# Kernel tuning notes

Hardware: AMD Instinct MI355X
Metric: run time of the kernel (lower is better)

Reference implementation:

```python
import jax, jax.numpy as jnp
import numpy as np

IGNORE = -100000.0


def setup_inputs() -> dict:
    key = jax.random.key(0)
    ks = jax.random.split(key, 5)
    b, s, d_model = 4, 2048, 2048
    n_q, n_kv, d_head = 32, 8, 64
    std = 0.02
    return {
        "normalized_resid_pre": jax.random.normal(ks[0], (b, s, d_model), jnp.float32),
        "W_Q": jax.random.normal(ks[1], (n_q, d_model, d_head), jnp.float32) * std,
        "W_K": jax.random.normal(ks[2], (n_kv, d_model, d_head), jnp.float32) * std,
        "W_V": jax.random.normal(ks[3], (n_kv, d_model, d_head), jnp.float32) * std,
        "W_O": jax.random.normal(ks[4], (n_kv, d_head, d_model), jnp.float32) * std,
    }


def reference(normalized_resid_pre, W_Q, W_K, W_V, W_O):
    x = normalized_resid_pre
    b, s, _ = x.shape
    n_kv, d_head = W_K.shape[0], W_K.shape[2]
    n_q = W_Q.shape[0]
    g = n_q // n_kv

    q = jnp.einsum("bpd,hdk->bphk", x, W_Q)  # [b,s,n_q,d_head]
    k = jnp.einsum("bpd,ndk->bpnk", x, W_K)  # [b,s,n_kv,d_head]
    v = jnp.einsum("bpd,ndk->bpnk", x, W_V)  # [b,s,n_kv,d_head]

    # rearrange: head axis splits as (n_kv_heads, g_size), then moved to [b,s,g,n_kv,d_head]
    gq = q.reshape(b, s, n_kv, g, d_head).transpose(0, 1, 3, 2, 4)

    # NOTE: faithful to source — g axis is SUMMED in this einsum
    scores = jnp.einsum("bqgnh,bknh->bnqk", gq, k) / jnp.sqrt(jnp.float32(d_head))

    causal = jnp.triu(jnp.ones((s, s), dtype=bool), k=1)  # True above diagonal
    scores = jnp.where(causal, IGNORE, scores)
    pattern = jax.nn.softmax(scores, axis=-1)  # [b,n_kv,q,k]

    z = jnp.einsum("bknh,bnqk->bqnh", v, pattern)  # [b,s,n_kv,d_head]
    attn_out = jnp.einsum("bqnh,nhd->bqd", z, W_O)  # [b,s,d_model]
    return attn_out
```

## Files before the change

### kernel.cpp

```cpp
#include <hip/hip_runtime.h>

typedef __attribute__((ext_vector_type(8))) _Float16 half8;
typedef __attribute__((ext_vector_type(4))) float f32x4;

#define BATCH  4
#define SLEN   2048
#define DMODEL 2048
#define NKV    8
#define GRP    4
#define DH     64
#define QKV    1536
#define KVDIM  512
#define MROWS  (BATCH * SLEN)

__device__ __forceinline__ unsigned short f2h(float f) {
    union { _Float16 h; unsigned short u; } cv;
    cv.h = (_Float16)f;
    return cv.u;
}

__device__ __forceinline__ void gl16(const void* g, void* l) {
    __builtin_amdgcn_global_load_lds(
        (const __attribute__((address_space(1))) void*)g,
        (__attribute__((address_space(3))) void*)l, 16, 0, 0);
}

typedef __attribute__((ext_vector_type(4))) short short4v;
union U64S4 { unsigned long long u; short4v s; };

__global__ __launch_bounds__(256) void k_packT(const float* __restrict__ wq,
                                               const float* __restrict__ wk,
                                               const float* __restrict__ wv,
                                               unsigned short* __restrict__ outT) {
    __shared__ float T[64][65];
    const int d0 = blockIdx.x * 64;
    const int ct = blockIdx.y;
    const int mat = ct >> 3, n = ct & 7;
    const int tr = threadIdx.x >> 6, tc = threadIdx.x & 63;
#pragma unroll
    for (int i = 0; i < 16; ++i) {
        int row = tr + i * 4;
        float v;
        if (mat == 0) {
            v = 0.0f;
#pragma unroll
            for (int g = 0; g < GRP; ++g)
                v += wq[((size_t)(n * GRP + g) * DMODEL + d0 + row) * DH + tc];
        } else if (mat == 1) {
            v = wk[((size_t)n * DMODEL + d0 + row) * DH + tc];
        } else {
            v = wv[((size_t)n * DMODEL + d0 + row) * DH + tc];
        }
        T[row][tc] = v;
    }
    __syncthreads();
    const int rr = tc;
#pragma unroll
    for (int i = 0; i < 16; ++i) {
        int cc = tr + i * 4;
        outT[(size_t)(mat * 512 + n * 64 + cc) * DMODEL + d0 + rr] = f2h(T[rr][cc]);
    }
}

__global__ __launch_bounds__(256) void k_transconv_h(const float* __restrict__ in,
                                                     unsigned short* __restrict__ outT,
                                                     int R, int C) {
    __shared__ float T[64][65];
    const int r0 = blockIdx.x * 64, c0 = blockIdx.y * 64;
    const int tr = threadIdx.x >> 6, tc = threadIdx.x & 63;
#pragma unroll
    for (int i = 0; i < 16; ++i)
        T[tr + i * 4][tc] = in[(size_t)(r0 + tr + i * 4) * C + c0 + tc];
    __syncthreads();
    const int rr = tc;
#pragma unroll
    for (int i = 0; i < 16; ++i) {
        int cc = tr + i * 4;
        outT[(size_t)(c0 + cc) * R + r0 + rr] = f2h(T[rr][cc]);
    }
}

__global__ __launch_bounds__(256) void k_convh(const float* __restrict__ in,
                                               unsigned short* __restrict__ out,
                                               int n4) {
    int i = blockIdx.x * 256 + threadIdx.x;
    if (i >= n4) return;
    float4 v = ((const float4*)in)[i];
    ushort4 o;
    o.x = f2h(v.x); o.y = f2h(v.y); o.z = f2h(v.z); o.w = f2h(v.w);
    ((ushort4*)out)[i] = o;
}

__device__ __forceinline__ void stage_rows(const unsigned short* __restrict__ src,
                                           unsigned short* lds, int t, int K,
                                           int k0, int nslots4) {
#pragma unroll
    for (int j = 0; j < 8; ++j) {
        if (j >= nslots4) break;
        int slot = j * 256 + t;
        int row = slot >> 3, blk = slot & 7;
        int c = blk ^ (row & 7);
        gl16(src + (size_t)row * K + k0 + c * 8, lds + slot * 8);
    }
}

__global__ __launch_bounds__(256) void k_gemm_qkv(
        const unsigned short* __restrict__ Ag, const unsigned short* __restrict__ Bg,
        unsigned short* __restrict__ qk, unsigned short* __restrict__ vT) {
    __shared__ unsigned short A2[2][128 * 64];
    __shared__ unsigned short B2[2][192 * 64];

    const int t = threadIdx.x;
    const size_t m0 = (size_t)blockIdx.x * 128, n0 = (size_t)blockIdx.y * 192;
    const int w = t >> 6, l = t & 63;
    const int wm = (w >> 1) * 64, wn = (w & 1) * 96;
    const int r = l & 15, q = l >> 4;
    f32x4 acc[4][6] = {};
    const int K = DMODEL;
    const int NT = K / 64;

    stage_rows(Ag + m0 * K, A2[0], t, K, 0, 4);
    stage_rows(Bg + n0 * K, B2[0], t, K, 0, 6);
    asm volatile("s_waitcnt vmcnt(0)" ::: "memory");
    __builtin_amdgcn_s_barrier();
    int cur = 0;
    for (int kt = 0; kt < NT; ++kt) {
        if (kt + 1 < NT) {
            stage_rows(Ag + m0 * K, A2[cur ^ 1], t, K, (kt + 1) * 64, 4);
            stage_rows(Bg + n0 * K, B2[cur ^ 1], t, K, (kt + 1) * 64, 6);
        }
        const unsigned short* Ac = A2[cur];
        const unsigned short* Bc = B2[cur];
        half8 af[4][2], bf[6][2];
#pragma unroll
        for (int i = 0; i < 4; ++i)
#pragma unroll
            for (int ks = 0; ks < 2; ++ks) {
                int ra = wm + i * 16 + r;
                af[i][ks] = *(const half8*)&Ac[ra * 64 + ((((ks << 2) | q) ^ (ra & 7)) << 3)];
            }
#pragma unroll
        for (int j = 0; j < 6; ++j)
#pragma unroll
            for (int ks = 0; ks < 2; ++ks) {
                int rb = wn + j * 16 + r;
                bf[j][ks] = *(const half8*)&Bc[rb * 64 + ((((ks << 2) | q) ^ (rb & 7)) << 3)];
            }
        __builtin_amdgcn_s_setprio(1);
#pragma unroll
        for (int i = 0; i < 4; ++i)
#pragma unroll
            for (int j = 0; j < 6; ++j) {
                acc[i][j] = __builtin_amdgcn_mfma_f32_16x16x32_f16(af[i][0], bf[j][0], acc[i][j], 0, 0, 0);
                acc[i][j] = __builtin_amdgcn_mfma_f32_16x16x32_f16(af[i][1], bf[j][1], acc[i][j], 0, 0, 0);
            }
        __builtin_amdgcn_s_setprio(0);
        asm volatile("s_waitcnt vmcnt(0)" ::: "memory");
        __builtin_amdgcn_s_barrier();
        cur ^= 1;
    }

#pragma unroll
    for (int i = 0; i < 4; ++i)
#pragma unroll
        for (int j = 0; j < 6; ++j) {
            int col = (int)n0 + wn + j * 16 + r;
            size_t rowb = m0 + wm + i * 16 + q * 4;
            if (col < 1024) {
#pragma unroll
                for (int e = 0; e < 4; ++e)
                    qk[(rowb + e) * 1024 + col] = f2h(acc[i][j][e]);
            } else {
                int d = col - 1024;
                ushort4 pk;
                pk.x = f2h(acc[i][j][0]); pk.y = f2h(acc[i][j][1]);
                pk.z = f2h(acc[i][j][2]); pk.w = f2h(acc[i][j][3]);
                *(ushort4*)&vT[(size_t)d * MROWS + rowb] = pk;
            }
        }
}

__global__ __launch_bounds__(256) void k_gemm_out(
        const unsigned short* __restrict__ Ag, const unsigned short* __restrict__ Bg,
        float* __restrict__ C) {
    __shared__ unsigned short A2[2][128 * 64];
    __shared__ unsigned short B2[2][128 * 64];

    const int t = threadIdx.x;
    const size_t m0 = (size_t)blockIdx.x * 128, n0 = (size_t)blockIdx.y * 128;
    const int w = t >> 6, l = t & 63;
    const int wm = (w >> 1) * 64, wn = (w & 1) * 64;
    const int r = l & 15, q = l >> 4;
    f32x4 acc[4][4] = {};
    const int K = KVDIM;
    const int NT = K / 64;

    stage_rows(Ag + m0 * K, A2[0], t, K, 0, 4);
    stage_rows(Bg + n0 * K, B2[0], t, K, 0, 4);
    asm volatile("s_waitcnt vmcnt(0)" ::: "memory");
    __builtin_amdgcn_s_barrier();
    int cur = 0;
    for (int kt = 0; kt < NT; ++kt) {
        if (kt + 1 < NT) {
            stage_rows(Ag + m0 * K, A2[cur ^ 1], t, K, (kt + 1) * 64, 4);
            stage_rows(Bg + n0 * K, B2[cur ^ 1], t, K, (kt + 1) * 64, 4);
        }
        const unsigned short* Ac = A2[cur];
        const unsigned short* Bc = B2[cur];
        half8 af[4][2], bf[4][2];
#pragma unroll
        for (int i = 0; i < 4; ++i)
#pragma unroll
            for (int ks = 0; ks < 2; ++ks) {
                int ra = wm + i * 16 + r;
                af[i][ks] = *(const half8*)&Ac[ra * 64 + ((((ks << 2) | q) ^ (ra & 7)) << 3)];
                int rb = wn + i * 16 + r;
                bf[i][ks] = *(const half8*)&Bc[rb * 64 + ((((ks << 2) | q) ^ (rb & 7)) << 3)];
            }
        __builtin_amdgcn_s_setprio(1);
#pragma unroll
        for (int i = 0; i < 4; ++i)
#pragma unroll
            for (int j = 0; j < 4; ++j) {
                acc[i][j] = __builtin_amdgcn_mfma_f32_16x16x32_f16(af[i][0], bf[j][0], acc[i][j], 0, 0, 0);
                acc[i][j] = __builtin_amdgcn_mfma_f32_16x16x32_f16(af[i][1], bf[j][1], acc[i][j], 0, 0, 0);
            }
        __builtin_amdgcn_s_setprio(0);
        asm volatile("s_waitcnt vmcnt(0)" ::: "memory");
        __builtin_amdgcn_s_barrier();
        cur ^= 1;
    }

#pragma unroll
    for (int i = 0; i < 4; ++i)
#pragma unroll
        for (int j = 0; j < 4; ++j) {
            int col = (int)n0 + wn + j * 16 + r;
            size_t rowb = m0 + wm + i * 16 + q * 4;
#pragma unroll
            for (int e = 0; e < 4; ++e)
                C[(rowb + e) * DMODEL + col] = acc[i][j][e];
        }
}

__global__ __launch_bounds__(256) void k_attn_mfma(
        const unsigned short* __restrict__ qk, const unsigned short* __restrict__ vT,
        unsigned short* __restrict__ zh) {
    __shared__ unsigned short Ks[2][128 * 64];
    __shared__ unsigned short Vs[2][64 * 128];
    __shared__ unsigned short Pt[4 * 128 * 16];

    const int t  = threadIdx.x;
    const int w  = t >> 6, l = t & 63;
    const int p  = blockIdx.x;
    const int n  = blockIdx.y, b = blockIdx.z;
    const int r  = l & 15, g = l >> 4;
    const int wq0 = w * 16;

#define STAGE_KV(buf, kr0)                                                    \
    _Pragma("unroll") for (int j2 = 0; j2 < 4; ++j2) {                        \
        int s2 = j2 * 256 + t;                                                \
        int rK = s2 >> 3, cK = (s2 & 7) ^ (rK & 7);                           \
        gl16(qk + ((kr0) + rK) * 1024 + 512 + n * 64 + cK * 8,                \
             &Ks[buf][s2 * 8]);                                               \
        int rV = s2 >> 4, cV = (s2 & 15) ^ (rV & 15);                         \
        gl16(vT + (size_t)(n * 64 + rV) * MROWS + (kr0) + cV * 8,             \
             &Vs[buf][s2 * 8]);                                               \
    }

#pragma unroll 1
    for (int seg = 0; seg < 2; ++seg) {
        const int qt = seg ? p : (31 - p);
        const int nkt = (qt + 2) >> 1;
        const size_t qrow0 = (size_t)(b * SLEN + qt * 64);

        half8 qh[2];
#pragma unroll
        for (int ks = 0; ks < 2; ++ks) {
            size_t off = (qrow0 + wq0 + r) * 1024 + n * 64 + ks * 32 + g * 8;
            qh[ks] = *(const half8*)(qk + off);
#pragma unroll
            for (int e2 = 0; e2 < 8; ++e2) qh[ks][e2] = qh[ks][e2] * (_Float16)0.125f;
        }

        STAGE_KV(0, (size_t)(b * SLEN))
        asm volatile("s_waitcnt vmcnt(0)" ::: "memory");
        __builtin_amdgcn_s_barrier();

        float m_[4], lsum[4];
#pragma unroll
        for (int e = 0; e < 4; ++e) { m_[e] = -3.0e38f; lsum[e] = 0.0f; }
        f32x4 accz[4] = {};

        for (int kt = 0; kt < nkt; ++kt) {
            const int cur = kt & 1;
            if (kt + 1 < nkt) {
                STAGE_KV(cur ^ 1, (size_t)(b * SLEN + (kt + 1) * 128))
            }
            const unsigned short* Ksc = Ks[cur];
            const unsigned short* Vsc = Vs[cur];

            f32x4 s[8] = {};
#pragma unroll
            for (int ct = 0; ct < 8; ++ct)
#pragma unroll
                for (int ks = 0; ks < 2; ++ks) {
                    int row = ct * 16 + r;
                    int off = row * 128 + (((ks * 4 + g) ^ (row & 7)) << 4);
                    half8 kh8 = *(const half8*)((char*)Ksc + off);
                    s[ct] = __builtin_amdgcn_mfma_f32_16x16x32_f16(qh[ks], kh8, s[ct], 0, 0, 0);
                }

            if (kt == nkt - 1) {
#pragma unroll
                for (int ct = 0; ct < 8; ++ct)
#pragma unroll
                    for (int e = 0; e < 4; ++e)
                        if ((kt * 128 + ct * 16 + r) > (qt * 64 + wq0 + g * 4 + e))
                            s[ct][e] = -100000.0f;
            }

            float al[4], nm[4];
#pragma unroll
            for (int e = 0; e < 4; ++e) {
                float pm = fmaxf(fmaxf(fmaxf(s[0][e], s[1][e]), fmaxf(s[2][e], s[3][e])),
                                 fmaxf(fmaxf(s[4][e], s[5][e]), fmaxf(s[6][e], s[7][e])));
                pm = fmaxf(pm, __shfl_xor(pm, 1));
                pm = fmaxf(pm, __shfl_xor(pm, 2));
                pm = fmaxf(pm, __shfl_xor(pm, 4));
                pm = fmaxf(pm, __shfl_xor(pm, 8));
                nm[e] = fmaxf(m_[e], pm);
                al[e] = __expf(m_[e] - nm[e]);
                m_[e] = nm[e];
            }
            {
                int src = (r >> 2) << 4;
                float a0 = __shfl(al[0], src), a1 = __shfl(al[1], src);
                float a2 = __shfl(al[2], src), a3 = __shfl(al[3], src);
                float ax = (r & 1) ? a1 : a0, ay = (r & 1) ? a3 : a2;
                float aq = (r & 2) ? ay : ax;
#pragma unroll
                for (int dt = 0; dt < 4; ++dt) {
                    accz[dt][0] *= aq; accz[dt][1] *= aq;
                    accz[dt][2] *= aq; accz[dt][3] *= aq;
                }
            }

            float ps[4] = {};
#pragma unroll
            for (int ct = 0; ct < 8; ++ct) {
                float p0 = __expf(s[ct][0] - m_[0]);
                float p1 = __expf(s[ct][1] - m_[1]);
                float p2 = __expf(s[ct][2] - m_[2]);
                float p3 = __expf(s[ct][3] - m_[3]);
                ps[0] += p0; ps[1] += p1; ps[2] += p2; ps[3] += p3;
                short4v pk = { (short)f2h(p0), (short)f2h(p1),
                               (short)f2h(p2), (short)f2h(p3) };
                int kv = ct * 16 + r;
                int phys = (kv >> 5) * 32 + (((kv >> 2) & 1) << 4)
                         + (((kv >> 3) & 3) << 2) + (kv & 3);
                *(short4v*)((char*)Pt + w * 4096 + phys * 32 + g * 8) = pk;
            }

#pragma unroll
            for (int e = 0; e < 4; ++e) {
                float rs = ps[e];
                rs += __shfl_xor(rs, 1); rs += __shfl_xor(rs, 2);
                rs += __shfl_xor(rs, 4); rs += __shfl_xor(rs, 8);
                lsum[e] = lsum[e] * al[e] + rs;
            }

            asm volatile("s_waitcnt lgkmcnt(0)" ::: "memory");
            __builtin_amdgcn_sched_barrier(0);
            U64S4 tA[4], tB[4];
#pragma unroll
            for (int ks = 0; ks < 4; ++ks) {
                unsigned base = (unsigned)(size_t)((char*)Pt + w * 4096 + ks * 1024) + l * 8;
                asm volatile("ds_read_b64_tr_b16 %0, %1" : "=v"(tA[ks].u) : "v"(base) : "memory");
                asm volatile("ds_read_b64_tr_b16 %0, %1" : "=v"(tB[ks].u) : "v"(base + 512) : "memory");
            }
            asm volatile("s_waitcnt lgkmcnt(0)" ::: "memory");
            __builtin_amdgcn_sched_barrier(0);
#pragma unroll
            for (int ks = 0; ks < 4; ++ks) {
                union { short s[8]; half8 h; } pf;
                pf.s[0] = tA[ks].s[0]; pf.s[1] = tA[ks].s[1];
                pf.s[2] = tA[ks].s[2]; pf.s[3] = tA[ks].s[3];
                pf.s[4] = tB[ks].s[0]; pf.s[5] = tB[ks].s[1];
                pf.s[6] = tB[ks].s[2]; pf.s[7] = tB[ks].s[3];
#pragma unroll
                for (int dt = 0; dt < 4; ++dt) {
                    int d = dt * 16 + r;
                    int off = d * 256 + (((ks * 4 + g) ^ (d & 15)) << 4);
                    half8 vfrag = *(const half8*)((char*)Vsc + off);
                    accz[dt] = __builtin_amdgcn_mfma_f32_16x16x32_f16(vfrag, pf.h, accz[dt], 0, 0, 0);
                }
            }

            asm volatile("s_waitcnt vmcnt(0)" ::: "memory");
            __builtin_amdgcn_s_barrier();
        }

        int src = (r >> 2) << 4;
        float l0 = __shfl(lsum[0], src), l1 = __shfl(lsum[1], src);
        float l2 = __shfl(lsum[2], src), l3 = __shfl(lsum[3], src);
        float lx = (r & 1) ? l1 : l0, ly = (r & 1) ? l3 : l2;
        float inv = 1.0f / ((r & 2) ? ly : lx);
#pragma unroll
        for (int dt = 0; dt < 4; ++dt) {
            ushort4 h4;
#pragma unroll
            for (int e = 0; e < 4; ++e)
                ((unsigned short*)&h4)[e] = f2h(accz[dt][e] * inv);
            size_t off = (qrow0 + wq0 + r) * 512 + n * 64 + dt * 16 + g * 4;
            *(ushort4*)(zh + off) = h4;
        }
    }
#undef STAGE_KV
}

extern "C" void kernel_launch(void* const* d_in, const int* in_sizes, int n_in,
                              void* d_out, int out_size, void* d_ws, size_t ws_size,
                              hipStream_t stream) {
    const float* x  = (const float*)d_in[0];
    const float* wq = (const float*)d_in[1];
    const float* wk = (const float*)d_in[2];
    const float* wv = (const float*)d_in[3];
    const float* wo = (const float*)d_in[4];
    float* out = (float*)d_out;

    char* w = (char*)d_ws;
    unsigned short* xh  = (unsigned short*)(w);
    unsigned short* zh  = (unsigned short*)(w);
    unsigned short* qk  = (unsigned short*)(w + 33554432);
    unsigned short* vT  = (unsigned short*)(w + 50331648);
    unsigned short* wcatT = (unsigned short*)(w + 58720256);
    unsigned short* woT = (unsigned short*)(w + 65011712);

    k_packT<<<dim3(32, 24), 256, 0, stream>>>(wq, wk, wv, wcatT);
    k_transconv_h<<<dim3(8, 32), 256, 0, stream>>>(wo, woT, KVDIM, DMODEL);
    k_convh<<<dim3(16384), 256, 0, stream>>>(x, xh, MROWS * DMODEL / 4);
    k_gemm_qkv<<<dim3(64, 8), 256, 0, stream>>>(xh, wcatT, qk, vT);
    k_attn_mfma<<<dim3(16, NKV, BATCH), 256, 0, stream>>>(qk, vT, zh);
    k_gemm_out<<<dim3(64, 16), 256, 0, stream>>>(zh, woT, out);
}
```

Before: 188.2 us.

## Double query rows per attention block to reuse staged K/V tiles

The attention kernel now processes 128 query rows per block instead of 64, with each wave handling two 16-row query slices against the same K/V tiles in LDS. This halves K/V staging traffic and barriers per query row, and the grid is halved to match. In exchange it doubles accumulator and score registers per wave, grows the P staging buffer, restricts occupancy to one block per SIMD set via launch bounds, and leaves fewer blocks for load balancing under the causal mask.

After: 200.5 us. +6.5%, slower.

```diff
diff --git a/kernel.cpp b/kernel.cpp
--- a/kernel.cpp
+++ b/kernel.cpp
@@ -243,19 +243,18 @@
         }
 }
 
-__global__ __launch_bounds__(256) void k_attn_mfma(
+__global__ __launch_bounds__(256, 1) void k_attn_mfma(
         const unsigned short* __restrict__ qk, const unsigned short* __restrict__ vT,
         unsigned short* __restrict__ zh) {
     __shared__ unsigned short Ks[2][128 * 64];
     __shared__ unsigned short Vs[2][64 * 128];
-    __shared__ unsigned short Pt[4 * 128 * 16];
+    __shared__ unsigned short Pt[4 * 2 * 2048];
 
     const int t  = threadIdx.x;
     const int w  = t >> 6, l = t & 63;
     const int p  = blockIdx.x;
     const int n  = blockIdx.y, b = blockIdx.z;
     const int r  = l & 15, g = l >> 4;
-    const int wq0 = w * 16;
 
 #define STAGE_KV(buf, kr0)                                                    \
     _Pragma("unroll") for (int j2 = 0; j2 < 4; ++j2) {                        \
@@ -270,27 +269,32 @@
 
 #pragma unroll 1
     for (int seg = 0; seg < 2; ++seg) {
-        const int qt = seg ? p : (31 - p);
-        const int nkt = (qt + 2) >> 1;
-        const size_t qrow0 = (size_t)(b * SLEN + qt * 64);
-
-        half8 qh[2];
-#pragma unroll
-        for (int ks = 0; ks < 2; ++ks) {
-            size_t off = (qrow0 + wq0 + r) * 1024 + n * 64 + ks * 32 + g * 8;
-            qh[ks] = *(const half8*)(qk + off);
-#pragma unroll
-            for (int e2 = 0; e2 < 8; ++e2) qh[ks][e2] = qh[ks][e2] * (_Float16)0.125f;
-        }
+        const int qt = seg ? p : (15 - p);
+        const int nkt = qt + 1;
+        const size_t qrow0 = (size_t)(b * SLEN + qt * 128);
+
+        half8 qh[2][2];
+#pragma unroll
+        for (int qs = 0; qs < 2; ++qs)
+#pragma unroll
+            for (int ks = 0; ks < 2; ++ks) {
+                size_t off = (qrow0 + w * 32 + qs * 16 + r) * 1024 + n * 64 + ks * 32 + g * 8;
+                qh[qs][ks] = *(const half8*)(qk + off);
+#pragma unroll
+                for (int e2 = 0; e2 < 8; ++e2)
+                    qh[qs][ks][e2] = qh[qs][ks][e2] * (_Float16)0.125f;
+            }
 
         STAGE_KV(0, (size_t)(b * SLEN))
         asm volatile("s_waitcnt vmcnt(0)" ::: "memory");
         __builtin_amdgcn_s_barrier();
 
-        float m_[4], lsum[4];
-#pragma unroll
-        for (int e = 0; e < 4; ++e) { m_[e] = -3.0e38f; lsum[e] = 0.0f; }
-        f32x4 accz[4] = {};
+        float m_[2][4], lsum[2][4];
+#pragma unroll
+        for (int qs = 0; qs < 2; ++qs)
+#pragma unroll
+            for (int e = 0; e < 4; ++e) { m_[qs][e] = -3.0e38f; lsum[qs][e] = 0.0f; }
+        f32x4 accz[2][4] = {};
 
         for (int kt = 0; kt < nkt; ++kt) {
             const int cur = kt & 1;
@@ -300,7 +304,7 @@
             const unsigned short* Ksc = Ks[cur];
             const unsigned short* Vsc = Vs[cur];
 
-            f32x4 s[8] = {};
+            f32x4 s[2][8] = {};
 #pragma unroll
             for (int ct = 0; ct < 8; ++ct)
 #pragma unroll
@@ -308,92 +312,103 @@
                     int row = ct * 16 + r;
                     int off = row * 128 + (((ks * 4 + g) ^ (row & 7)) << 4);
                     half8 kh8 = *(const half8*)((char*)Ksc + off);
-                    s[ct] = __builtin_amdgcn_mfma_f32_16x16x32_f16(qh[ks], kh8, s[ct], 0, 0, 0);
+                    s[0][ct] = __builtin_amdgcn_mfma_f32_16x16x32_f16(qh[0][ks], kh8, s[0][ct], 0, 0, 0);
+                    s[1][ct] = __builtin_amdgcn_mfma_f32_16x16x32_f16(qh[1][ks], kh8, s[1][ct], 0, 0, 0);
                 }
 
             if (kt == nkt - 1) {
 #pragma unroll
-                for (int ct = 0; ct < 8; ++ct)
-#pragma unroll
-                    for (int e = 0; e < 4; ++e)
-                        if ((kt * 128 + ct * 16 + r) > (qt * 64 + wq0 + g * 4 + e))
-                            s[ct][e] = -100000.0f;
-            }
-
-            float al[4], nm[4];
-#pragma unroll
-            for (int e = 0; e < 4; ++e) {
-                float pm = fmaxf(fmaxf(fmaxf(s[0][e], s[1][e]), fmaxf(s[2][e], s[3][e])),
-                                 fmaxf(fmaxf(s[4][e], s[5][e]), fmaxf(s[6][e], s[7][e])));
-                pm = fmaxf(pm, __shfl_xor(pm, 1));
-                pm = fmaxf(pm, __shfl_xor(pm, 2));
-                pm = fmaxf(pm, __shfl_xor(pm, 4));
-                pm = fmaxf(pm, __shfl_xor(pm, 8));
-                nm[e] = fmaxf(m_[e], pm);
-                al[e] = __expf(m_[e] - nm[e]);
-                m_[e] = nm[e];
-            }
-            {
-                int src = (r >> 2) << 4;
-                float a0 = __shfl(al[0], src), a1 = __shfl(al[1], src);
-                float a2 = __shfl(al[2], src), a3 = __shfl(al[3], src);
-                float ax = (r & 1) ? a1 : a0, ay = (r & 1) ? a3 : a2;
-                float aq = (r & 2) ? ay : ax;
-#pragma unroll
-                for (int dt = 0; dt < 4; ++dt) {
-                    accz[dt][0] *= aq; accz[dt][1] *= aq;
-                    accz[dt][2] *= aq; accz[dt][3] *= aq;
-                }
-            }
-
-            float ps[4] = {};
-#pragma unroll
-            for (int ct = 0; ct < 8; ++ct) {
-                float p0 = __expf(s[ct][0] - m_[0]);
-                float p1 = __expf(s[ct][1] - m_[1]);
-                float p2 = __expf(s[ct][2] - m_[2]);
-                float p3 = __expf(s[ct][3] - m_[3]);
-                ps[0] += p0; ps[1] += p1; ps[2] += p2; ps[3] += p3;
-                short4v pk = { (short)f2h(p0), (short)f2h(p1),
-                               (short)f2h(p2), (short)f2h(p3) };
-                int kv = ct * 16 + r;
-                int phys = (kv >> 5) * 32 + (((kv >> 2) & 1) << 4)
-                         + (((kv >> 3) & 3) << 2) + (kv & 3);
-                *(short4v*)((char*)Pt + w * 4096 + phys * 32 + g * 8) = pk;
-            }
-
-#pragma unroll
-            for (int e = 0; e < 4; ++e) {
-                float rs = ps[e];
-                rs += __shfl_xor(rs, 1); rs += __shfl_xor(rs, 2);
-                rs += __shfl_xor(rs, 4); rs += __shfl_xor(rs, 8);
-                lsum[e] = lsum[e] * al[e] + rs;
+                for (int qs = 0; qs < 2; ++qs)
+#pragma unroll
+                    for (int ct = 0; ct < 8; ++ct)
+#pragma unroll
+                        for (int e = 0; e < 4; ++e)
+                            if ((kt * 128 + ct * 16 + r) >
+                                (qt * 128 + w * 32 + qs * 16 + g * 4 + e))
+                                s[qs][ct][e] = -100000.0f;
+            }
+
+#pragma unroll
+            for (int qs = 0; qs < 2; ++qs) {
+                float al[4];
+#pragma unroll
+                for (int e = 0; e < 4; ++e) {
+                    float pm = fmaxf(fmaxf(fmaxf(s[qs][0][e], s[qs][1][e]), fmaxf(s[qs][2][e], s[qs][3][e])),
+                                     fmaxf(fmaxf(s[qs][4][e], s[qs][5][e]), fmaxf(s[qs][6][e], s[qs][7][e])));
+                    pm = fmaxf(pm, __shfl_xor(pm, 1));
+                    pm = fmaxf(pm, __shfl_xor(pm, 2));
+                    pm = fmaxf(pm, __shfl_xor(pm, 4));
+                    pm = fmaxf(pm, __shfl_xor(pm, 8));
+                    float nm = fmaxf(m_[qs][e], pm);
+                    al[e] = __expf(m_[qs][e] - nm);
+                    m_[qs][e] = nm;
+                }
+                {
+                    int src = (r >> 2) << 4;
+                    float a0 = __shfl(al[0], src), a1 = __shfl(al[1], src);
+                    float a2 = __shfl(al[2], src), a3 = __shfl(al[3], src);
+                    float ax = (r & 1) ? a1 : a0, ay = (r & 1) ? a3 : a2;
+                    float aq = (r & 2) ? ay : ax;
+#pragma unroll
+                    for (int dt = 0; dt < 4; ++dt) {
+                        accz[qs][dt][0] *= aq; accz[qs][dt][1] *= aq;
+                        accz[qs][dt][2] *= aq; accz[qs][dt][3] *= aq;
+                    }
+                }
+
+                float ps[4] = {};
+#pragma unroll
+                for (int ct = 0; ct < 8; ++ct) {
+                    float p0 = __expf(s[qs][ct][0] - m_[qs][0]);
+                    float p1 = __expf(s[qs][ct][1] - m_[qs][1]);
+                    float p2 = __expf(s[qs][ct][2] - m_[qs][2]);
+                    float p3 = __expf(s[qs][ct][3] - m_[qs][3]);
+                    ps[0] += p0; ps[1] += p1; ps[2] += p2; ps[3] += p3;
+                    short4v pk = { (short)f2h(p0), (short)f2h(p1),
+                                   (short)f2h(p2), (short)f2h(p3) };
+                    int kv = ct * 16 + r;
+                    int phys = (kv >> 5) * 32 + (((kv >> 2) & 1) << 4)
+                             + (((kv >> 3) & 3) << 2) + (kv & 3);
+                    *(short4v*)((char*)Pt + (w * 2 + qs) * 4096 + phys * 32 + g * 8) = pk;
+                }
+
+#pragma unroll
+                for (int e = 0; e < 4; ++e) {
+                    float rs = ps[e];
+                    rs += __shfl_xor(rs, 1); rs += __shfl_xor(rs, 2);
+                    rs += __shfl_xor(rs, 4); rs += __shfl_xor(rs, 8);
+                    lsum[qs][e] = lsum[qs][e] * al[e] + rs;
+                }
             }
 
             asm volatile("s_waitcnt lgkmcnt(0)" ::: "memory");
             __builtin_amdgcn_sched_barrier(0);
-            U64S4 tA[4], tB[4];
-#pragma unroll
-            for (int ks = 0; ks < 4; ++ks) {
-                unsigned base = (unsigned)(size_t)((char*)Pt + w * 4096 + ks * 1024) + l * 8;
-                asm volatile("ds_read_b64_tr_b16 %0, %1" : "=v"(tA[ks].u) : "v"(base) : "memory");
-                asm volatile("ds_read_b64_tr_b16 %0, %1" : "=v"(tB[ks].u) : "v"(base + 512) : "memory");
-            }
+            U64S4 tA[2][4], tB[2][4];
+#pragma unroll
+            for (int qs = 0; qs < 2; ++qs)
+#pragma unroll
+                for (int ks = 0; ks < 4; ++ks) {
+                    unsigned base = (unsigned)(size_t)((char*)Pt + (w * 2 + qs) * 4096 + ks * 1024) + l * 8;
+                    asm volatile("ds_read_b64_tr_b16 %0, %1" : "=v"(tA[qs][ks].u) : "v"(base) : "memory");
+                    asm volatile("ds_read_b64_tr_b16 %0, %1" : "=v"(tB[qs][ks].u) : "v"(base + 512) : "memory");
+                }
             asm volatile("s_waitcnt lgkmcnt(0)" ::: "memory");
             __builtin_amdgcn_sched_barrier(0);
 #pragma unroll
             for (int ks = 0; ks < 4; ++ks) {
-                union { short s[8]; half8 h; } pf;
-                pf.s[0] = tA[ks].s[0]; pf.s[1] = tA[ks].s[1];
-                pf.s[2] = tA[ks].s[2]; pf.s[3] = tA[ks].s[3];
-                pf.s[4] = tB[ks].s[0]; pf.s[5] = tB[ks].s[1];
-                pf.s[6] = tB[ks].s[2]; pf.s[7] = tB[ks].s[3];
+                union { short s[8]; half8 h; } pf0, pf1;
+#pragma unroll
+                for (int e2 = 0; e2 < 4; ++e2) {
+                    pf0.s[e2] = tA[0][ks].s[e2]; pf0.s[4 + e2] = tB[0][ks].s[e2];
+                    pf1.s[e2] = tA[1][ks].s[e2]; pf1.s[4 + e2] = tB[1][ks].s[e2];
+                }
 #pragma unroll
                 for (int dt = 0; dt < 4; ++dt) {
                     int d = dt * 16 + r;
                     int off = d * 256 + (((ks * 4 + g) ^ (d & 15)) << 4);
                     half8 vfrag = *(const half8*)((char*)Vsc + off);
-                    accz[dt] = __builtin_amdgcn_mfma_f32_16x16x32_f16(vfrag, pf.h, accz[dt], 0, 0, 0);
+                    accz[0][dt] = __builtin_amdgcn_mfma_f32_16x16x32_f16(vfrag, pf0.h, accz[0][dt], 0, 0, 0);
+                    accz[1][dt] = __builtin_amdgcn_mfma_f32_16x16x32_f16(vfrag, pf1.h, accz[1][dt], 0, 0, 0);
                 }
             }
 
@@ -401,19 +416,22 @@
             __builtin_amdgcn_s_barrier();
         }
 
-        int src = (r >> 2) << 4;
-        float l0 = __shfl(lsum[0], src), l1 = __shfl(lsum[1], src);
-        float l2 = __shfl(lsum[2], src), l3 = __shfl(lsum[3], src);
-        float lx = (r & 1) ? l1 : l0, ly = (r & 1) ? l3 : l2;
-        float inv = 1.0f / ((r & 2) ? ly : lx);
-#pragma unroll
-        for (int dt = 0; dt < 4; ++dt) {
-            ushort4 h4;
-#pragma unroll
-            for (int e = 0; e < 4; ++e)
-                ((unsigned short*)&h4)[e] = f2h(accz[dt][e] * inv);
-            size_t off = (qrow0 + wq0 + r) * 512 + n * 64 + dt * 16 + g * 4;
-            *(ushort4*)(zh + off) = h4;
+#pragma unroll
+        for (int qs = 0; qs < 2; ++qs) {
+            int src = (r >> 2) << 4;
+            float l0 = __shfl(lsum[qs][0], src), l1 = __shfl(lsum[qs][1], src);
+            float l2 = __shfl(lsum[qs][2], src), l3 = __shfl(lsum[qs][3], src);
+            float lx = (r & 1) ? l1 : l0, ly = (r & 1) ? l3 : l2;
+            float inv = 1.0f / ((r & 2) ? ly : lx);
+#pragma unroll
+            for (int dt = 0; dt < 4; ++dt) {
+                ushort4 h4;
+#pragma unroll
+                for (int e = 0; e < 4; ++e)
+                    ((unsigned short*)&h4)[e] = f2h(accz[qs][dt][e] * inv);
+                size_t off = (qrow0 + w * 32 + qs * 16 + r) * 512 + n * 64 + dt * 16 + g * 4;
+                *(ushort4*)(zh + off) = h4;
+            }
         }
     }
 #undef STAGE_KV
@@ -441,6 +459,6 @@
     k_transconv_h<<<dim3(8, 32), 256, 0, stream>>>(wo, woT, KVDIM, DMODEL);
     k_convh<<<dim3(16384), 256, 0, stream>>>(x, xh, MROWS * DMODEL / 4);
     k_gemm_qkv<<<dim3(64, 8), 256, 0, stream>>>(xh, wcatT, qk, vT);
-    k_attn_mfma<<<dim3(16, NKV, BATCH), 256, 0, stream>>>(qk, vT, zh);
+    k_attn_mfma<<<dim3(8, NKV, BATCH), 256, 0, stream>>>(qk, vT, zh);
     k_gemm_out<<<dim3(64, 16), 256, 0, stream>>>(zh, woT, out);
 }
```
